# Kernel optimization log

Hardware: AMD Instinct MI355X
Metric: run time of the kernel (lower is better)

The kernel has to match this reference:

```python
import jax, jax.numpy as jnp
import numpy as np
from jax.ops import segment_sum, segment_max

N = 100000   # nodes
E = 1600000  # edges
B = 256      # graphs
H = 128      # hidden_channels
F_IN = 4     # input_size
EPS = 1e-5


def _graph_norm(x, w, b, ms, batch):
    # PyG GraphNorm: out = w * (x - ms*mean_g) / sqrt(var_g + eps) + b
    cnt = jnp.maximum(segment_sum(jnp.ones((x.shape[0],), x.dtype), batch, num_segments=B), 1.0)
    mean = segment_sum(x, batch, num_segments=B) / cnt[:, None]
    out = x - mean[batch] * ms
    var = segment_sum(out * out, batch, num_segments=B) / cnt[:, None]
    return w * out / jnp.sqrt(var + EPS)[batch] + b


def _gcn(x, W, b, src, dst):
    # GCNConv with self-loops and symmetric normalization (src/dst already include self-loops)
    h = x @ W                                              # [N, H]
    deg = segment_sum(jnp.ones_like(src, dtype=h.dtype), dst, num_segments=N)
    dinv = jax.lax.rsqrt(jnp.maximum(deg, 1.0))
    norm = dinv[src] * dinv[dst]                           # [E+N]
    return segment_sum(norm[:, None] * h[src], dst, num_segments=N) + b


def _seg_softmax(gate, batch):
    gmax = segment_max(gate, batch, num_segments=B)
    e = jnp.exp(gate - gmax[batch])
    den = segment_sum(e, batch, num_segments=B)
    return e / den[batch]


def setup_inputs() -> dict:
    key = jax.random.key(0)
    ks = jax.random.split(key, 16)
    x = jax.random.normal(ks[0], (N, F_IN), jnp.float32)
    edge_index = jax.random.randint(ks[1], (2, E), 0, N, dtype=jnp.int64)
    batch = jnp.sort(jax.random.randint(ks[2], (N,), 0, B, dtype=jnp.int64))
    r = lambda k, shp, fan: jax.random.normal(k, shp, jnp.float32) / np.sqrt(fan)
    inp = {
        "x": x, "edge_index": edge_index, "batch": batch,
        "W1": r(ks[3], (F_IN, H), F_IN), "b1": jnp.zeros((H,), jnp.float32),
        "W2": r(ks[4], (H, H), H), "b2": jnp.zeros((H,), jnp.float32),
        "W3": r(ks[5], (H, H), H), "b3": jnp.zeros((H,), jnp.float32),
        "gn0_w": jnp.ones((F_IN,), jnp.float32), "gn0_b": jnp.zeros((F_IN,), jnp.float32), "gn0_ms": jnp.ones((F_IN,), jnp.float32),
        "gn1_w": jnp.ones((H,), jnp.float32), "gn1_b": jnp.zeros((H,), jnp.float32), "gn1_ms": jnp.ones((H,), jnp.float32),
        "gn2_w": jnp.ones((H,), jnp.float32), "gn2_b": jnp.zeros((H,), jnp.float32), "gn2_ms": jnp.ones((H,), jnp.float32),
        "gn3_w": jnp.ones((H,), jnp.float32), "gn3_b": jnp.zeros((H,), jnp.float32), "gn3_ms": jnp.ones((H,), jnp.float32),
        "g1": r(ks[6], (H, H), H), "gb1": jnp.zeros((H,), jnp.float32),
        "g2": r(ks[7], (H, H), H), "gb2": jnp.zeros((H,), jnp.float32),
        "g3": r(ks[8], (H, 1), H), "gb3": jnp.zeros((1,), jnp.float32),
        "l1": r(ks[9], (H, H), H), "lb1": jnp.zeros((H,), jnp.float32),
        "l2": r(ks[10], (H, H), H), "lb2": jnp.zeros((H,), jnp.float32),
        "l3": r(ks[11], (H, 1), H), "lb3": jnp.zeros((1,), jnp.float32),
    }
    return inp


def reference(x, edge_index, batch, W1, b1, W2, b2, W3, b3,
              gn0_w, gn0_b, gn0_ms, gn1_w, gn1_b, gn1_ms,
              gn2_w, gn2_b, gn2_ms, gn3_w, gn3_b, gn3_ms,
              g1, gb1, g2, gb2, g3, gb3,
              l1, lb1, l2, lb2, l3, lb3):
    loop = jnp.arange(N, dtype=edge_index.dtype)
    src = jnp.concatenate([edge_index[0], loop])
    dst = jnp.concatenate([edge_index[1], loop])

    h = _graph_norm(x, gn0_w, gn0_b, gn0_ms, batch)
    h = _gcn(h, W1, b1, src, dst)
    h = jax.nn.relu(_graph_norm(h, gn1_w, gn1_b, gn1_ms, batch))
    h = _gcn(h, W2, b2, src, dst)
    h = jax.nn.relu(_graph_norm(h, gn2_w, gn2_b, gn2_ms, batch))
    h = _gcn(h, W3, b3, src, dst)
    h = _graph_norm(h, gn3_w, gn3_b, gn3_ms, batch)

    # GlobalAttention: gate_nn -> scalar gate per node, segment softmax, weighted sum
    g = jax.nn.relu(h @ g1 + gb1)
    g = jax.nn.relu(g @ g2 + gb2)
    gate = g @ g3 + gb3                                   # [N, 1]
    attn = _seg_softmax(gate, batch)                      # [N, 1]
    pooled = segment_sum(attn * h, batch, num_segments=B) # [B, H]

    o = jax.nn.relu(pooled @ l1 + lb1)
    o = jax.nn.relu(o @ l2 + lb2)
    return o @ l3 + lb3                                   # [B, 1]
```

## Files before the change

kernel.cpp:

```cpp
#include <hip/hip_runtime.h>
#include <hip/hip_bf16.h>

#define NN 100000
#define NE 1600000
#define NB 256
#define HD 128
#define EPS 1e-5f
#define NBUK 1563
#define SLOTB 1536
#define EPB 8192
#define NCHK 8

typedef __attribute__((ext_vector_type(8))) short bf16x8v;
typedef __attribute__((ext_vector_type(4))) float f32x4v;

__device__ __forceinline__ float rd_dyn(const void* p, int i, int fflag) {
    if (fflag) {
        unsigned short u = ((const unsigned short*)p)[i];
        return __uint_as_float(((unsigned)u) << 16);
    }
    return ((const float*)p)[i];
}

__device__ __forceinline__ int rd_idx(const int* p, int k, int iflag) {
    return iflag ? p[k] : p[2 * k];
}

__device__ __forceinline__ unsigned short f2bf(float v) {
    __hip_bfloat16 b = __float2bfloat16(v);
    return *(unsigned short*)&b;
}

__device__ __forceinline__ float bflo(unsigned u) { return __uint_as_float(u << 16); }
__device__ __forceinline__ float bfhi(unsigned u) { return __uint_as_float(u & 0xFFFF0000u); }
__device__ __forceinline__ unsigned packbf(float a, float b) {
    return (unsigned)f2bf(a) | ((unsigned)f2bf(b) << 16);
}

__global__ void k_mark7(unsigned short* __restrict__ out, int n) {
    int i = blockIdx.x * blockDim.x + threadIdx.x;
    if (i < n) out[i] = 0x40E0;
}

__global__ void k_init(const unsigned* __restrict__ w, int* __restrict__ flags) {
    if (threadIdx.x == 0 && blockIdx.x == 0) {
        flags[0] = 0;
        flags[1] = (w[0] == 0x3F803F80u) ? 1 : 0;
    }
}

__global__ void k_detect(const int* __restrict__ w, int* __restrict__ iflag, int n) {
    int i = blockIdx.x * blockDim.x + threadIdx.x;
    if (i < n && (i & 1) && w[i] != 0) atomicOr(iflag, 1);
}

struct CvtArgs {
    const void* p[30];
    int n[30];
    int off[30];
};
__global__ void k_cvtf_all(CvtArgs a, float* __restrict__ out, const int* __restrict__ fflagp) {
    int j = blockIdx.y;
    int i = blockIdx.x * blockDim.x + threadIdx.x;
    if (i >= a.n[j]) return;
    out[a.off[j] + i] = rd_dyn(a.p[j], i, *fflagp);
}

__global__ void k_transp(const float* __restrict__ P, int o0, int o1, int o2, int o3,
                         unsigned short* __restrict__ WT) {
    int mat = blockIdx.y;
    int off = mat == 0 ? o0 : mat == 1 ? o1 : mat == 2 ? o2 : o3;
    int i = blockIdx.x * 256 + threadIdx.x;
    int nidx = i >> 7, k = i & 127;
    WT[mat * 16384 + nidx * 128 + k] = f2bf(P[off + k * 128 + nidx]);
}

__global__ void k_start(const int* __restrict__ batch, const int* __restrict__ iflagp,
                        int* __restrict__ start, int* __restrict__ batch32,
                        int* __restrict__ bcur, int n) {
    int i = blockIdx.x * blockDim.x + threadIdx.x;
    if (i >= n) return;
    if (i < NBUK) bcur[i] = i * SLOTB;
    int ifl = *iflagp;
    int b = rd_idx(batch, i, ifl); b = b < 0 ? 0 : (b > NB - 1 ? NB - 1 : b);
    batch32[i] = b;
    int bp;
    if (i == 0) bp = -1;
    else { bp = rd_idx(batch, i - 1, ifl); bp = bp < 0 ? 0 : (bp > NB - 1 ? NB - 1 : bp); }
    for (int g = bp + 1; g <= b; ++g) start[g] = i;
    if (i == n - 1) { for (int g = b + 1; g <= NB; ++g) start[g] = n; }
}

__global__ __launch_bounds__(256) void k_bfill(const int* __restrict__ ei,
                                               const int* __restrict__ iflagp,
                                               int* __restrict__ bcur,
                                               unsigned* __restrict__ bkte, int e) {
    __shared__ int lh[NBUK];
    __shared__ int lbase[NBUK];
    int ifl = *iflagp;
    for (int b = threadIdx.x; b < NBUK; b += 256) lh[b] = 0;
    __syncthreads();
    int s0 = blockIdx.x * EPB;
    int s1 = s0 + EPB; if (s1 > e) s1 = e;
    for (int i = s0 + threadIdx.x; i < s1; i += 256) {
        int d = rd_idx(ei, NE + i, ifl);
        int s = rd_idx(ei, i, ifl);
        if ((unsigned)d < (unsigned)NN && (unsigned)s < (unsigned)NN)
            atomicAdd(&lh[d >> 6], 1);
    }
    __syncthreads();
    for (int b = threadIdx.x; b < NBUK; b += 256) {
        int c = lh[b];
        if (c) { lbase[b] = atomicAdd(&bcur[b], c); lh[b] = 0; }
    }
    __syncthreads();
    for (int i = s0 + threadIdx.x; i < s1; i += 256) {
        int d = rd_idx(ei, NE + i, ifl);
        int s = rd_idx(ei, i, ifl);
        if ((unsigned)d < (unsigned)NN && (unsigned)s < (unsigned)NN) {
            int b = d >> 6;
            int li = atomicAdd(&lh[b], 1);
            bkte[lbase[b] + li] = ((unsigned)s << 6) | (unsigned)(d & 63);
        }
    }
}

__global__ __launch_bounds__(256) void k_csrfin(const unsigned* __restrict__ bkte,
                                                const int* __restrict__ bcur,
                                                int* __restrict__ rowptr,
                                                int* __restrict__ cnt,
                                                float* __restrict__ dinv,
                                                int* __restrict__ esrc) {
    __shared__ int lc[64];
    __shared__ int lcur[64];
    int b = blockIdx.x, t = threadIdx.x;
    int base = b * 64;
    if (t < 64) lc[t] = 0;
    __syncthreads();
    int r0 = b * SLOTB, r1 = bcur[b];
    for (int j = r0 + t; j < r1; j += 256)
        atomicAdd(&lc[(int)(bkte[j] & 63u)], 1);
    __syncthreads();
    if (t < 64) {
        int v = lc[t];
        int inc = v;
#pragma unroll
        for (int off = 1; off < 64; off <<= 1) {
            int nv = __shfl_up(inc, off, 64);
            if (t >= off) inc += nv;
        }
        int ex = r0 + inc - v;
        lcur[t] = ex;
        int node = base + t;
        if (node < NN) {
            rowptr[node] = ex;
            cnt[node] = v;
            dinv[node] = rsqrtf((float)(v + 1));
        }
    }
    __syncthreads();
    for (int j = r0 + t; j < r1; j += 256) {
        unsigned p = bkte[j];
        int slot = atomicAdd(&lcur[p & 63u], 1);
        esrc[slot] = (int)(p >> 6);
    }
}

__global__ __launch_bounds__(64) void k_gn4(const void* __restrict__ x,
                                            const float* __restrict__ w,
                                            const float* __restrict__ bb,
                                            const float* __restrict__ ms,
                                            const int* __restrict__ start,
                                            const int* __restrict__ fflagp,
                                            float* __restrict__ out) {
    int g = blockIdx.x;
    int s0 = start[g], s1 = start[g + 1];
    if (s1 <= s0) return;
    int ff = *fflagp;
    float cnt = (float)(s1 - s0);
    int t = threadIdx.x;
    int c = t & 3, p = t >> 2;
    __shared__ float reds[64], redq[64];
    float s = 0.f, q = 0.f;
    for (int n = s0 + p; n < s1; n += 16) {
        float v = rd_dyn(x, n * 4 + c, ff);
        s += v; q = fmaf(v, v, q);
    }
    reds[t] = s; redq[t] = q; __syncthreads();
    for (int off = 8; off >= 1; off >>= 1) {
        if (p < off) { reds[t] += reds[t + 4 * off]; redq[t] += redq[t + 4 * off]; }
        __syncthreads();
    }
    float mean = reds[c] / cnt;
    float sq = redq[c] / cnt;
    float sub = mean * ms[c];
    float var = sq - 2.f * sub * mean + sub * sub;
    float scale = w[c] * rsqrtf(var + EPS);
    float bias = bb[c];
    for (int n = s0 + p; n < s1; n += 16) {
        float d = rd_dyn(x, n * 4 + c, ff) - sub;
        out[n * 4 + c] = scale * d + bias;
    }
}

__global__ __launch_bounds__(256) void k_gnstats_part(const unsigned* __restrict__ Xu,
                                                      const int* __restrict__ start,
                                                      float* __restrict__ PS,
                                                      float* __restrict__ PQ) {
    int g = blockIdx.x, k = blockIdx.y;
    int s0 = start[g], s1 = start[g + 1];
    int len = (s1 - s0 + NCHK - 1) / NCHK;
    int c0 = s0 + k * len, c1 = c0 + len; if (c1 > s1) c1 = s1;
    int t = threadIdx.x;
    int cp = t & 63, p = t >> 6;
    __shared__ float r0s[256], r1s[256], r0q[256], r1q[256];
    float s0a = 0.f, s1a = 0.f, q0a = 0.f, q1a = 0.f;
    for (int n = c0 + p; n < c1; n += 4) {
        unsigned u = Xu[n * 64 + cp];
        float lo = bflo(u), hi = bfhi(u);
        s0a += lo; q0a = fmaf(lo, lo, q0a);
        s1a += hi; q1a = fmaf(hi, hi, q1a);
    }
    r0s[t] = s0a; r1s[t] = s1a; r0q[t] = q0a; r1q[t] = q1a;
    __syncthreads();
    if (p == 0) {
        float a0 = r0s[cp] + r0s[64 + cp] + r0s[128 + cp] + r0s[192 + cp];
        float a1 = r1s[cp] + r1s[64 + cp] + r1s[128 + cp] + r1s[192 + cp];
        float b0 = r0q[cp] + r0q[64 + cp] + r0q[128 + cp] + r0q[192 + cp];
        float b1 = r1q[cp] + r1q[64 + cp] + r1q[128 + cp] + r1q[192 + cp];
        int bidx = (g * NCHK + k) * 128;
        PS[bidx + 2 * cp] = a0; PS[bidx + 2 * cp + 1] = a1;
        PQ[bidx + 2 * cp] = b0; PQ[bidx + 2 * cp + 1] = b1;
    }
}

__global__ __launch_bounds__(128) void k_gnstats_final(const float* __restrict__ PS,
                                                       const float* __restrict__ PQ,
                                                       const float* __restrict__ w,
                                                       const float* __restrict__ ms,
                                                       const int* __restrict__ start,
                                                       float* __restrict__ SUB,
                                                       float* __restrict__ SCALE) {
    int g = blockIdx.x, c = threadIdx.x;
    int n = start[g + 1] - start[g];
    if (n <= 0) return;
    float cnt = (float)n;
    float s = 0.f, q = 0.f;
#pragma unroll
    for (int k = 0; k < NCHK; ++k) {
        s += PS[(g * NCHK + k) * 128 + c];
        q += PQ[(g * NCHK + k) * 128 + c];
    }
    float mean = s / cnt;
    float sq = q / cnt;
    float sub = mean * ms[c];
    float var = sq - 2.f * sub * mean + sub * sub;
    SUB[g * 128 + c] = sub;
    SCALE[g * 128 + c] = w[c] * rsqrtf(var + EPS);
}

__global__ __launch_bounds__(256) void k_gather4gemm(const int* __restrict__ rowptr,
                                                     const int* __restrict__ cnt,
                                                     const int* __restrict__ esrc,
                                                     const float* __restrict__ dinv,
                                                     const float* __restrict__ h0,
                                                     const float* __restrict__ W1,
                                                     const float* __restrict__ b1,
                                                     unsigned* __restrict__ Xu) {
    __shared__ float w1s[512];
    __shared__ float b1s[128];
    int tid = threadIdx.x;
    w1s[tid] = W1[tid];
    w1s[256 + tid] = W1[256 + tid];
    if (tid < 128) b1s[tid] = b1[tid];
    __syncthreads();
    int node = blockIdx.x * 4 + (tid >> 6);
    int lane = tid & 63;
    if (node >= NN) return;
    int ch = lane & 3;
    int r0 = rowptr[node], r1 = r0 + cnt[node];
    double acc = 0.0;
    for (int j = r0 + (lane >> 2); j < r1; j += 16) {
        int s = esrc[j];
        acc += (double)(dinv[s] * h0[s * 4 + ch]);
    }
#pragma unroll
    for (int mask = 4; mask <= 32; mask <<= 1)
        acc += __shfl_xor(acc, mask, 64);
    float dd = dinv[node];
    float z = (float)(dd * acc) + dd * dd * h0[node * 4 + ch];
    float za = __shfl(z, 0, 64), zb = __shfl(z, 1, 64);
    float zc = __shfl(z, 2, 64), zd = __shfl(z, 3, 64);
    int c0 = 2 * lane, c1 = 2 * lane + 1;
    float v0 = za * w1s[c0] + zb * w1s[128 + c0] + zc * w1s[256 + c0] + zd * w1s[384 + c0] + b1s[c0];
    float v1 = za * w1s[c1] + zb * w1s[128 + c1] + zc * w1s[256 + c1] + zd * w1s[384 + c1] + b1s[c1];
    Xu[node * 64 + lane] = packbf(v0, v1);
}

__global__ __launch_bounds__(256) void k_gemm_mfma_bf(const unsigned* __restrict__ Xu,
                                                      const int* __restrict__ batch32,
                                                      const float* __restrict__ SUB,
                                                      const float* __restrict__ SCALE,
                                                      const float* __restrict__ gnb,
                                                      int relu,
                                                      const unsigned short* __restrict__ WT,
                                                      const float* __restrict__ dinv,
                                                      unsigned short* __restrict__ out) {
    __shared__ unsigned short xs[16][136];
    int base = blockIdx.x * 16;
    int tid = threadIdx.x;
    for (int idx = tid; idx < 1024; idx += 256) {
        int r = idx >> 6, cp = idx & 63;
        int g = batch32[base + r];
        unsigned u = Xu[(base + r) * 64 + cp];
        float2 sub = ((const float2*)(SUB + g * 128))[cp];
        float2 sc  = ((const float2*)(SCALE + g * 128))[cp];
        float2 gb  = ((const float2*)gnb)[cp];
        float va = (bflo(u) - sub.x) * sc.x + gb.x;
        float vb = (bfhi(u) - sub.y) * sc.y + gb.y;
        if (relu) { va = fmaxf(va, 0.f); vb = fmaxf(vb, 0.f); }
        xs[r][2 * cp] = f2bf(va);
        xs[r][2 * cp + 1] = f2bf(vb);
    }
    __syncthreads();
    int wave = tid >> 6, lane = tid & 63;
    int m = lane & 15, quad = lane >> 4;
    f32x4v acc0 = {0.f, 0.f, 0.f, 0.f}, acc1 = {0.f, 0.f, 0.f, 0.f};
    int c0 = wave * 32 + m, c1 = c0 + 16;
#pragma unroll
    for (int kk = 0; kk < 4; ++kk) {
        int ko = kk * 32 + quad * 8;
        bf16x8v a  = *(const bf16x8v*)&xs[m][ko];
        bf16x8v b0 = *(const bf16x8v*)&WT[c0 * 128 + ko];
        bf16x8v b1 = *(const bf16x8v*)&WT[c1 * 128 + ko];
        acc0 = __builtin_amdgcn_mfma_f32_16x16x32_bf16(a, b0, acc0, 0, 0, 0);
        acc1 = __builtin_amdgcn_mfma_f32_16x16x32_bf16(a, b1, acc1, 0, 0, 0);
    }
#pragma unroll
    for (int reg = 0; reg < 4; ++reg) {
        int row = base + quad * 4 + reg;
        float dv = dinv[row];
        out[row * 128 + c0] = f2bf(dv * acc0[reg]);
        out[row * 128 + c1] = f2bf(dv * acc1[reg]);
    }
}

__global__ __launch_bounds__(256) void k_gather_bf(const int* __restrict__ rowptr,
                                                   const int* __restrict__ cnt,
                                                   const int* __restrict__ esrc,
                                                   const float* __restrict__ dinv,
                                                   const unsigned* __restrict__ h,
                                                   const float* __restrict__ bias,
                                                   unsigned* __restrict__ Xu) {
    int node = blockIdx.x * 4 + (threadIdx.x >> 6);
    int lane = threadIdx.x & 63;
    if (node >= NN) return;
    int r0 = rowptr[node], r1 = r0 + cnt[node];
    double ax = 0.0, ay = 0.0;
    int j = r0;
    for (; j + 7 < r1; j += 8) {
        unsigned u[8];
#pragma unroll
        for (int q = 0; q < 8; ++q) u[q] = h[esrc[j + q] * 64 + lane];
#pragma unroll
        for (int q = 0; q < 8; ++q) {
            ax += (double)bflo(u[q]);
            ay += (double)bfhi(u[q]);
        }
    }
    for (; j < r1; ++j) {
        unsigned u = h[esrc[j] * 64 + lane];
        ax += (double)bflo(u);
        ay += (double)bfhi(u);
    }
    float dd = dinv[node];
    unsigned us = h[node * 64 + lane];
    float2 bb = ((const float2*)bias)[lane];
    float ox = dd * ((float)ax + bflo(us)) + bb.x;
    float oy = dd * ((float)ay + bfhi(us)) + bb.y;
    Xu[node * 64 + lane] = packbf(ox, oy);
}

__global__ __launch_bounds__(256) void k_gate_fused(const unsigned* __restrict__ Xu,
                                                    const int* __restrict__ batch32,
                                                    const float* __restrict__ SUB,
                                                    const float* __restrict__ SCALE,
                                                    const float* __restrict__ gnb,
                                                    const unsigned short* __restrict__ GT1,
                                                    const float* __restrict__ gb1,
                                                    const unsigned short* __restrict__ GT2,
                                                    const float* __restrict__ gb2,
                                                    const float* __restrict__ g3,
                                                    const float* __restrict__ gb3,
                                                    float* __restrict__ gate) {
    __shared__ unsigned short xs[16][136];
    __shared__ unsigned short t1[16][136];
    __shared__ float redw[64];
    int base = blockIdx.x * 16;
    int tid = threadIdx.x;
    for (int idx = tid; idx < 1024; idx += 256) {
        int r = idx >> 6, cp = idx & 63;
        int g = batch32[base + r];
        unsigned u = Xu[(base + r) * 64 + cp];
        float2 sub = ((const float2*)(SUB + g * 128))[cp];
        float2 sc  = ((const float2*)(SCALE + g * 128))[cp];
        float2 gb  = ((const float2*)gnb)[cp];
        xs[r][2 * cp] = f2bf((bflo(u) - sub.x) * sc.x + gb.x);
        xs[r][2 * cp + 1] = f2bf((bfhi(u) - sub.y) * sc.y + gb.y);
    }
    __syncthreads();
    int wave = tid >> 6, lane = tid & 63;
    int m = lane & 15, quad = lane >> 4;
    int c0 = wave * 32 + m, c1 = c0 + 16;
    f32x4v acc0 = {0.f, 0.f, 0.f, 0.f}, acc1 = {0.f, 0.f, 0.f, 0.f};
#pragma unroll
    for (int kk = 0; kk < 4; ++kk) {
        int ko = kk * 32 + quad * 8;
        bf16x8v a  = *(const bf16x8v*)&xs[m][ko];
        bf16x8v b0 = *(const bf16x8v*)&GT1[c0 * 128 + ko];
        bf16x8v b1 = *(const bf16x8v*)&GT1[c1 * 128 + ko];
        acc0 = __builtin_amdgcn_mfma_f32_16x16x32_bf16(a, b0, acc0, 0, 0, 0);
        acc1 = __builtin_amdgcn_mfma_f32_16x16x32_bf16(a, b1, acc1, 0, 0, 0);
    }
    float bj0 = gb1[c0], bj1 = gb1[c1];
#pragma unroll
    for (int reg = 0; reg < 4; ++reg) {
        int row = quad * 4 + reg;
        t1[row][c0] = f2bf(fmaxf(acc0[reg] + bj0, 0.f));
        t1[row][c1] = f2bf(fmaxf(acc1[reg] + bj1, 0.f));
    }
    __syncthreads();
    f32x4v d0 = {0.f, 0.f, 0.f, 0.f}, d1 = {0.f, 0.f, 0.f, 0.f};
#pragma unroll
    for (int kk = 0; kk < 4; ++kk) {
        int ko = kk * 32 + quad * 8;
        bf16x8v a  = *(const bf16x8v*)&t1[m][ko];
        bf16x8v b0 = *(const bf16x8v*)&GT2[c0 * 128 + ko];
        bf16x8v b1 = *(const bf16x8v*)&GT2[c1 * 128 + ko];
        d0 = __builtin_amdgcn_mfma_f32_16x16x32_bf16(a, b0, d0, 0, 0, 0);
        d1 = __builtin_amdgcn_mfma_f32_16x16x32_bf16(a, b1, d1, 0, 0, 0);
    }
    float g30 = g3[c0], g31 = g3[c1];
    float bk0 = gb2[c0], bk1 = gb2[c1];
    float contrib[4];
#pragma unroll
    for (int reg = 0; reg < 4; ++reg) {
        float v0 = fmaxf(d0[reg] + bk0, 0.f);
        float v1 = fmaxf(d1[reg] + bk1, 0.f);
        contrib[reg] = v0 * g30 + v1 * g31;
    }
#pragma unroll
    for (int mask = 1; mask <= 8; mask <<= 1) {
#pragma unroll
        for (int reg = 0; reg < 4; ++reg)
            contrib[reg] += __shfl_xor(contrib[reg], mask, 64);
    }
    if (m == 0) {
#pragma unroll
        for (int reg = 0; reg < 4; ++reg)
            redw[wave * 16 + quad * 4 + reg] = contrib[reg];
    }
    __syncthreads();
    if (tid < 16) {
        float s = redw[tid] + redw[16 + tid] + redw[32 + tid] + redw[48 + tid];
        gate[base + tid] = s + gb3[0];
    }
}

__global__ __launch_bounds__(256) void k_smstats(const float* __restrict__ gate,
                                                 const int* __restrict__ start,
                                                 float2* __restrict__ SM) {
    int g = blockIdx.x;
    int s0 = start[g], s1 = start[g + 1];
    int t = threadIdx.x;
    __shared__ float red[256];
    if (s1 <= s0) { if (t == 0) SM[g] = make_float2(0.f, 1.f); return; }
    float m = -1e30f;
    for (int i = s0 + t; i < s1; i += 256) m = fmaxf(m, gate[i]);
    red[t] = m; __syncthreads();
    for (int off = 128; off; off >>= 1) { if (t < off) red[t] = fmaxf(red[t], red[t + off]); __syncthreads(); }
    m = red[0]; __syncthreads();
    float s = 0.f;
    for (int i = s0 + t; i < s1; i += 256) s += expf(gate[i] - m);
    red[t] = s; __syncthreads();
    for (int off = 128; off; off >>= 1) { if (t < off) red[t] += red[t + off]; __syncthreads(); }
    if (t == 0) SM[g] = make_float2(m, red[0]);
}

__global__ __launch_bounds__(256) void k_pool_part(const unsigned* __restrict__ Xu,
                                                   const float* __restrict__ SUB,
                                                   const float* __restrict__ SCALE,
                                                   const float* __restrict__ gnb,
                                                   const float* __restrict__ gate,
                                                   const float2* __restrict__ SM,
                                                   const int* __restrict__ start,
                                                   float* __restrict__ PP) {
    int g = blockIdx.x, k = blockIdx.y;
    int s0 = start[g], s1 = start[g + 1];
    int len = (s1 - s0 + NCHK - 1) / NCHK;
    int c0 = s0 + k * len, c1 = c0 + len; if (c1 > s1) c1 = s1;
    int t = threadIdx.x, cp = t & 63, p = t >> 6;
    __shared__ float r0s[256], r1s[256];
    float2 sm = SM[g];
    float invden = 1.f / sm.y;
    float2 sub = ((const float2*)(SUB + g * 128))[cp];
    float2 sc  = ((const float2*)(SCALE + g * 128))[cp];
    float2 gb  = ((const float2*)gnb)[cp];
    float sa = 0.f, sb = 0.f;
    for (int n = c0 + p; n < c1; n += 4) {
        float a = expf(gate[n] - sm.x) * invden;
        unsigned u = Xu[n * 64 + cp];
        sa += a * ((bflo(u) - sub.x) * sc.x + gb.x);
        sb += a * ((bfhi(u) - sub.y) * sc.y + gb.y);
    }
    r0s[t] = sa; r1s[t] = sb; __syncthreads();
    if (p == 0) {
        int bidx = (g * NCHK + k) * 128;
        float2 o;
        o.x = r0s[cp] + r0s[64 + cp] + r0s[128 + cp] + r0s[192 + cp];
        o.y = r1s[cp] + r1s[64 + cp] + r1s[128 + cp] + r1s[192 + cp];
        ((float2*)(PP + bidx))[cp] = o;
    }
}

__global__ __launch_bounds__(128) void k_head(const float* __restrict__ PP,
                                              const float* __restrict__ l1, const float* __restrict__ lb1,
                                              const float* __restrict__ l2, const float* __restrict__ lb2,
                                              const float* __restrict__ l3, const float* __restrict__ lb3,
                                              const int* __restrict__ fflagp,
                                              void* __restrict__ out) {
    int g = blockIdx.x, t = threadIdx.x;
    __shared__ float p[128], o[128], red[128];
    float s = 0.f;
#pragma unroll
    for (int k = 0; k < NCHK; ++k) s += PP[(g * NCHK + k) * 128 + t];
    p[t] = s; __syncthreads();
    float a = 0.f;
    for (int k = 0; k < 128; ++k) a += p[k] * l1[k * 128 + t];
    a = fmaxf(a + lb1[t], 0.f);
    o[t] = a; __syncthreads();
    float b = 0.f;
    for (int k = 0; k < 128; ++k) b += o[k] * l2[k * 128 + t];
    b = fmaxf(b + lb2[t], 0.f);
    red[t] = b * l3[t]; __syncthreads();
    for (int off = 64; off; off >>= 1) { if (t < off) red[t] += red[t + off]; __syncthreads(); }
    if (t == 0) {
        float r = red[0] + lb3[0];
        if (*fflagp) ((__hip_bfloat16*)out)[g] = __float2bfloat16(r);
        else ((float*)out)[g] = r;
    }
}

extern "C" void kernel_launch(void* const* d_in, const int* in_sizes, int n_in,
                              void* d_out, int out_size, void* d_ws, size_t ws_size,
                              hipStream_t stream) {
    const void* x = d_in[0];
    const int* ei_raw = (const int*)d_in[1];
    const int* batch_raw = (const int*)d_in[2];
    (void)n_in; (void)out_size;

    char* ws = (char*)d_ws;
    size_t off = 0;
    auto alloc = [&](size_t bytes) -> void* {
        void* p = ws + off;
        off += (bytes + 255) & ~(size_t)255;
        return p;
    };
    unsigned* Xu  = (unsigned*)alloc((size_t)NN * HD * 2);
    float* Y      = (float*)alloc((size_t)NN * HD * 4);
    float* h0     = (float*)alloc((size_t)NN * 4 * 4);
    float* dinv   = (float*)alloc((size_t)NN * 4);
    float* gate   = (float*)alloc((size_t)NN * 4);
    int*   start  = (int*)alloc((size_t)(NB + 1) * 4);
    int*   batch32= (int*)alloc((size_t)NN * 4);
    float* P      = (float*)alloc((size_t)131072 * 4);
    unsigned short* WT = (unsigned short*)alloc((size_t)4 * 16384 * 2);
    float* SUB    = (float*)alloc((size_t)NB * HD * 4);
    float* SCALE  = (float*)alloc((size_t)NB * HD * 4);
    float* PS     = (float*)alloc((size_t)NB * NCHK * 128 * 4);
    float* PQ     = (float*)alloc((size_t)NB * NCHK * 128 * 4);
    float2* SM    = (float2*)alloc((size_t)NB * 8);
    int*   flags  = (int*)alloc(256);
    int*   rowptr = (int*)alloc((size_t)NN * 4);
    int*   cnt    = (int*)alloc((size_t)NN * 4);
    int*   esrc   = (int*)alloc((size_t)NBUK * SLOTB * 4);
    int*   bcur   = (int*)alloc((size_t)NBUK * 4);
    unsigned* bkte = (unsigned*)(Y + (size_t)NN * HD / 2);
    float* PP = PS;

    if (ws_size < off) {
        k_mark7<<<1, 256, 0, stream>>>((unsigned short*)d_out, NB);
        return;
    }

    int* iflag = flags;
    int* fflag = flags + 1;
    k_init<<<1, 64, 0, stream>>>((const unsigned*)d_in[12], flags);
    k_detect<<<(NN + 255) / 256, 256, 0, stream>>>(batch_raw, iflag, NN);

    CvtArgs ca;
    float* fp[33];
    int maxn = 1;
    {
        int poff = 0;
        for (int i = 3; i < 33; ++i) {
            int n = in_sizes[i];
            ca.p[i - 3] = d_in[i];
            ca.n[i - 3] = n;
            ca.off[i - 3] = poff;
            fp[i] = P + poff;
            poff += n;
            if (n > maxn) maxn = n;
        }
    }
    {
        dim3 grid((maxn + 255) / 256, 30);
        k_cvtf_all<<<grid, 256, 0, stream>>>(ca, P, fflag);
    }
    const float *W1 = fp[3], *b1 = fp[4], *b2 = fp[6], *b3 = fp[8];
    const float *gn0w = fp[9],  *gn0b = fp[10], *gn0m = fp[11];
    const float *gn1w = fp[12], *gn1b = fp[13], *gn1m = fp[14];
    const float *gn2w = fp[15], *gn2b = fp[16], *gn2m = fp[17];
    const float *gn3w = fp[18], *gn3b = fp[19], *gn3m = fp[20];
    const float *gb1 = fp[22], *gb2 = fp[24], *g3 = fp[25], *gb3 = fp[26];
    const float *l1 = fp[27], *lb1 = fp[28], *l2 = fp[29], *lb2 = fp[30], *l3 = fp[31], *lb3 = fp[32];

    {
        dim3 grid(64, 4);
        k_transp<<<grid, 256, 0, stream>>>(P, (int)(fp[5] - P), (int)(fp[7] - P),
                                           (int)(fp[21] - P), (int)(fp[23] - P), WT);
    }
    const unsigned short* WT2 = WT;
    const unsigned short* WT3 = WT + 16384;
    const unsigned short* GT1 = WT + 2 * 16384;
    const unsigned short* GT2 = WT + 3 * 16384;

    k_start<<<(NN + 255) / 256, 256, 0, stream>>>(batch_raw, iflag, start, batch32, bcur, NN);

    int ebg = (NE + EPB - 1) / EPB;
    k_bfill<<<ebg, 256, 0, stream>>>(ei_raw, iflag, bcur, bkte, NE);
    k_csrfin<<<NBUK, 256, 0, stream>>>(bkte, bcur, rowptr, cnt, dinv, esrc);

    k_gn4<<<NB, 64, 0, stream>>>(x, gn0w, gn0b, gn0m, start, fflag, h0);

    k_gather4gemm<<<(NN + 3) / 4, 256, 0, stream>>>(rowptr, cnt, esrc, dinv, h0, W1, b1, Xu);

    unsigned short* Yb = (unsigned short*)Y;
    dim3 sgrid(NB, NCHK);

    k_gnstats_part<<<sgrid, 256, 0, stream>>>(Xu, start, PS, PQ);
    k_gnstats_final<<<NB, 128, 0, stream>>>(PS, PQ, gn1w, gn1m, start, SUB, SCALE);
    k_gemm_mfma_bf<<<NN / 16, 256, 0, stream>>>(Xu, batch32, SUB, SCALE, gn1b, 1, WT2, dinv, Yb);
    k_gather_bf<<<(NN + 3) / 4, 256, 0, stream>>>(rowptr, cnt, esrc, dinv, (const unsigned*)Yb, b2, Xu);

    k_gnstats_part<<<sgrid, 256, 0, stream>>>(Xu, start, PS, PQ);
    k_gnstats_final<<<NB, 128, 0, stream>>>(PS, PQ, gn2w, gn2m, start, SUB, SCALE);
    k_gemm_mfma_bf<<<NN / 16, 256, 0, stream>>>(Xu, batch32, SUB, SCALE, gn2b, 1, WT3, dinv, Yb);
    k_gather_bf<<<(NN + 3) / 4, 256, 0, stream>>>(rowptr, cnt, esrc, dinv, (const unsigned*)Yb, b3, Xu);

    k_gnstats_part<<<sgrid, 256, 0, stream>>>(Xu, start, PS, PQ);
    k_gnstats_final<<<NB, 128, 0, stream>>>(PS, PQ, gn3w, gn3m, start, SUB, SCALE);
    k_gate_fused<<<NN / 16, 256, 0, stream>>>(Xu, batch32, SUB, SCALE, gn3b,
                                              GT1, gb1, GT2, gb2, g3, gb3, gate);
    k_smstats<<<NB, 256, 0, stream>>>(gate, start, SM);
    k_pool_part<<<sgrid, 256, 0, stream>>>(Xu, SUB, SCALE, gn3b, gate, SM, start, PP);
    k_head<<<NB, 128, 0, stream>>>(PP, l1, lb1, l2, lb2, l3, lb3, fflag, d_out);
}
```

Before: 567.5 us.

## Use fp32 accumulation and 16-byte vectorized edge gathers in GCN aggregation

Replaces double-precision accumulation with fp32 in both the first-layer aggregation and the bf16 gather kernel, avoiding slow FP64 adds. The gather kernel is restructured so that each wavefront processes four edges at once, with each lane loading a uint4 (8 bf16 values) per edge. Partial sums are then combined with cross-lane shuffles and written back in a permuted channel order. This trades some summation accuracy and extra shuffle work for fewer, wider memory transactions and more memory-level parallelism.

```diff
diff --git a/kernel.cpp b/kernel.cpp
--- a/kernel.cpp
+++ b/kernel.cpp
@@ -279,16 +279,16 @@
     if (node >= NN) return;
     int ch = lane & 3;
     int r0 = rowptr[node], r1 = r0 + cnt[node];
-    double acc = 0.0;
+    float acc = 0.f;
     for (int j = r0 + (lane >> 2); j < r1; j += 16) {
         int s = esrc[j];
-        acc += (double)(dinv[s] * h0[s * 4 + ch]);
+        acc += dinv[s] * h0[s * 4 + ch];
     }
 #pragma unroll
     for (int mask = 4; mask <= 32; mask <<= 1)
         acc += __shfl_xor(acc, mask, 64);
     float dd = dinv[node];
-    float z = (float)(dd * acc) + dd * dd * h0[node * 4 + ch];
+    float z = dd * acc + dd * dd * h0[node * 4 + ch];
     float za = __shfl(z, 0, 64), zb = __shfl(z, 1, 64);
     float zc = __shfl(z, 2, 64), zd = __shfl(z, 3, 64);
     int c0 = 2 * lane, c1 = 2 * lane + 1;
@@ -345,6 +345,12 @@
     }
 }
 
+#define ACC4(u) do { \
+    a0 += bflo((u).x); a1 += bfhi((u).x); \
+    a2 += bflo((u).y); a3 += bfhi((u).y); \
+    a4 += bflo((u).z); a5 += bfhi((u).z); \
+    a6 += bflo((u).w); a7 += bfhi((u).w); } while (0)
+
 __global__ __launch_bounds__(256) void k_gather_bf(const int* __restrict__ rowptr,
                                                    const int* __restrict__ cnt,
                                                    const int* __restrict__ esrc,
@@ -355,30 +361,48 @@
     int node = blockIdx.x * 4 + (threadIdx.x >> 6);
     int lane = threadIdx.x & 63;
     if (node >= NN) return;
+    int q = lane >> 4, s = lane & 15;
     int r0 = rowptr[node], r1 = r0 + cnt[node];
-    double ax = 0.0, ay = 0.0;
-    int j = r0;
-    for (; j + 7 < r1; j += 8) {
-        unsigned u[8];
-#pragma unroll
-        for (int q = 0; q < 8; ++q) u[q] = h[esrc[j + q] * 64 + lane];
-#pragma unroll
-        for (int q = 0; q < 8; ++q) {
-            ax += (double)bflo(u[q]);
-            ay += (double)bfhi(u[q]);
-        }
-    }
-    for (; j < r1; ++j) {
-        unsigned u = h[esrc[j] * 64 + lane];
-        ax += (double)bflo(u);
-        ay += (double)bfhi(u);
-    }
+    const uint4* hp = (const uint4*)h;
+    float a0 = 0.f, a1 = 0.f, a2 = 0.f, a3 = 0.f;
+    float a4 = 0.f, a5 = 0.f, a6 = 0.f, a7 = 0.f;
+    int j = r0 + q;
+    for (; j + 12 < r1; j += 16) {
+        int e0 = esrc[j], e1 = esrc[j + 4], e2 = esrc[j + 8], e3 = esrc[j + 12];
+        uint4 u0 = hp[e0 * 16 + s];
+        uint4 u1 = hp[e1 * 16 + s];
+        uint4 u2 = hp[e2 * 16 + s];
+        uint4 u3 = hp[e3 * 16 + s];
+        ACC4(u0); ACC4(u1); ACC4(u2); ACC4(u3);
+    }
+    for (; j + 4 < r1; j += 8) {
+        int e0 = esrc[j], e1 = esrc[j + 4];
+        uint4 u0 = hp[e0 * 16 + s];
+        uint4 u1 = hp[e1 * 16 + s];
+        ACC4(u0); ACC4(u1);
+    }
+    for (; j < r1; j += 4) {
+        int e0 = esrc[j];
+        uint4 u0 = hp[e0 * 16 + s];
+        ACC4(u0);
+    }
+    a0 += __shfl_xor(a0, 16, 64); a0 += __shfl_xor(a0, 32, 64);
+    a1 += __shfl_xor(a1, 16, 64); a1 += __shfl_xor(a1, 32, 64);
+    a2 += __shfl_xor(a2, 16, 64); a2 += __shfl_xor(a2, 32, 64);
+    a3 += __shfl_xor(a3, 16, 64); a3 += __shfl_xor(a3, 32, 64);
+    a4 += __shfl_xor(a4, 16, 64); a4 += __shfl_xor(a4, 32, 64);
+    a5 += __shfl_xor(a5, 16, 64); a5 += __shfl_xor(a5, 32, 64);
+    a6 += __shfl_xor(a6, 16, 64); a6 += __shfl_xor(a6, 32, 64);
+    a7 += __shfl_xor(a7, 16, 64); a7 += __shfl_xor(a7, 32, 64);
+    int cp = 4 * s + q;
+    float ax = q == 0 ? a0 : q == 1 ? a2 : q == 2 ? a4 : a6;
+    float ay = q == 0 ? a1 : q == 1 ? a3 : q == 2 ? a5 : a7;
     float dd = dinv[node];
-    unsigned us = h[node * 64 + lane];
-    float2 bb = ((const float2*)bias)[lane];
-    float ox = dd * ((float)ax + bflo(us)) + bb.x;
-    float oy = dd * ((float)ay + bfhi(us)) + bb.y;
-    Xu[node * 64 + lane] = packbf(ox, oy);
+    unsigned us = h[node * 64 + cp];
+    float2 bb = ((const float2*)bias)[cp];
+    float ox = dd * (ax + bflo(us)) + bb.x;
+    float oy = dd * (ay + bfhi(us)) + bb.y;
+    Xu[node * 64 + cp] = packbf(ox, oy);
 }
 
 __global__ __launch_bounds__(256) void k_gate_fused(const unsigned* __restrict__ Xu,
```

Measured after the change: 540.1 us. 4.8% less time.
